# Optimization experiments

Measured on AMD Instinct MI355X. Metric: run time of the kernel, lower is better.

The kernel has to match this reference:

```python
import jax, jax.numpy as jnp
import numpy as np

B, S, D = 2, 2048, 2048
H, KVH = 16, 4
HD = D // H            # 128
KVD = KVH * HD         # 512
ROPE_BASE = 10000.0
EPS = 1e-6


def setup_inputs() -> dict:
    key = jax.random.key(0)
    k0, k1, k2, k3, k4, k5 = jax.random.split(key, 6)
    x = jax.random.normal(k0, (B, S, D), dtype=jnp.float32)
    # torch Linear weights are [out_features, in_features]
    Wq = jax.random.normal(k1, (D, D), dtype=jnp.float32) * 0.02
    Wk = jax.random.normal(k2, (KVD, D), dtype=jnp.float32) * 0.02
    Wv = jax.random.normal(k3, (KVD, D), dtype=jnp.float32) * 0.02
    Wproj = jax.random.normal(k4, (D, D), dtype=jnp.float32) * 0.02
    q_gain = jnp.ones((H,), dtype=jnp.float32)
    return {"x": x, "Wq": Wq, "Wk": Wk, "Wv": Wv, "Wproj": Wproj, "q_gain": q_gain}


def _rms_norm(t):
    return t * jax.lax.rsqrt(jnp.mean(t * t, axis=-1, keepdims=True) + EPS)


def _rope_tables(seqlen, dtype):
    half = HD // 2
    inv_freq = 1.0 / (ROPE_BASE ** (jnp.arange(0, HD, 2, dtype=jnp.float32) / HD))
    freqs = jnp.outer(jnp.arange(seqlen, dtype=jnp.float32), inv_freq)  # [S, half]
    return jnp.cos(freqs).astype(dtype)[None, None], jnp.sin(freqs).astype(dtype)[None, None]


def _apply_rope(t, cos, sin):
    half = t.shape[-1] // 2
    t1, t2 = t[..., :half], t[..., half:]
    return jnp.concatenate((t1 * cos + t2 * sin, -t1 * sin + t2 * cos), axis=-1)


def reference(x, Wq, Wk, Wv, Wproj, q_gain):
    bsz, seqlen, _ = x.shape
    # QKV projections (F.linear: x @ W.T)
    q = jnp.einsum('bsd,ed->bse', x, Wq).reshape(bsz, seqlen, H, HD).transpose(0, 2, 1, 3)
    k = jnp.einsum('bsd,ed->bse', x, Wk).reshape(bsz, seqlen, KVH, HD).transpose(0, 2, 1, 3)
    v = jnp.einsum('bsd,ed->bse', x, Wv).reshape(bsz, seqlen, KVH, HD).transpose(0, 2, 1, 3)
    # QK RMS-norm
    q = _rms_norm(q)
    k = _rms_norm(k)
    # RoPE
    cos, sin = _rope_tables(seqlen, q.dtype)
    q = _apply_rope(q, cos, sin)
    k = _apply_rope(k, cos, sin)
    # per-head query gain
    q = q * q_gain.astype(q.dtype)[None, :, None, None]
    # GQA: repeat_interleave kv heads
    rep = H // KVH
    k = jnp.repeat(k, rep, axis=1)
    v = jnp.repeat(v, rep, axis=1)
    # causal SDPA
    scale = 1.0 / jnp.sqrt(jnp.asarray(HD, dtype=q.dtype))
    scores = jnp.einsum('bhqd,bhkd->bhqk', q, k) * scale
    causal = jnp.tril(jnp.ones((seqlen, seqlen), dtype=bool))
    scores = jnp.where(causal[None, None], scores, jnp.finfo(scores.dtype).min)
    attn = jax.nn.softmax(scores, axis=-1)
    y = jnp.einsum('bhqk,bhkd->bhqd', attn, v)
    y = y.transpose(0, 2, 1, 3).reshape(bsz, seqlen, H * HD)
    return jnp.einsum('bse,de->bsd', y, Wproj)
```

## Files before the change

kernel.cpp:

```cpp
#include <hip/hip_runtime.h>


typedef __bf16 bf16x8 __attribute__((ext_vector_type(8)));
typedef float  f32x4  __attribute__((ext_vector_type(4)));
typedef float  f32x16 __attribute__((ext_vector_type(16)));

#define LOG2E 1.4426950408889634f
#define FIXC  16.59099297022308f

__device__ __forceinline__ float b2f(ushort h) {
  return __builtin_bit_cast(float, ((unsigned)h) << 16);
}
__device__ __forceinline__ ushort f2b(float f) {
  unsigned u = __builtin_bit_cast(unsigned, f);
  return (ushort)((u + 0x7fffu + ((u >> 16) & 1u)) >> 16);
}
__device__ __forceinline__ void async16(ushort* lds, const ushort* g) {
  __builtin_amdgcn_global_load_lds(
      (const __attribute__((address_space(1))) unsigned int*)(const void*)g,
      (__attribute__((address_space(3))) unsigned int*)(void*)lds, 16, 0, 0);
}
__device__ __forceinline__ f32x4 mfma16(bf16x8 a, bf16x8 b, f32x4 c) {
  return __builtin_amdgcn_mfma_f32_16x16x32_bf16(a, b, c, 0, 0, 0);
}
__device__ __forceinline__ f32x16 mfma32(bf16x8 a, bf16x8 b, f32x16 c) {
  return __builtin_amdgcn_mfma_f32_32x32x16_bf16(a, b, c, 0, 0, 0);
}

__global__ __launch_bounds__(256) void castk(const float* __restrict__ in,
                                             ushort* __restrict__ out) {
  int i = blockIdx.x * 256 + threadIdx.x;
  float4 v = ((const float4*)in)[i];
  ushort4 o = make_ushort4(f2b(v.x), f2b(v.y), f2b(v.z), f2b(v.w));
  ((ushort4*)out)[i] = o;
}

__global__ void rope_tables(float* __restrict__ cosT, float* __restrict__ sinT) {
  int s = blockIdx.x;
  int i = threadIdx.x;
  float invf = exp2f(-(float)i * (13.287712379549449f / 64.0f));
  float ang = (float)s * invf;
  float sn, cs;
  sincosf(ang, &sn, &cs);
  cosT[s * 64 + i] = cs;
  sinT[s * 64 + i] = sn;
}

__device__ __forceinline__ void store_c(float* C, size_t idx, float v) { C[idx] = v; }
__device__ __forceinline__ void store_c(ushort* C, size_t idx, float v) { C[idx] = f2b(v); }

template <typename TOUT>
__global__ __launch_bounds__(256) void gemm_bt(const ushort* __restrict__ A,
                                               const ushort* __restrict__ Bw,
                                               TOUT* __restrict__ C,
                                               int M, int N, int K) {
  __shared__ __align__(16) ushort As[128 * 64];
  __shared__ __align__(16) ushort Bs[128 * 64];
  int tid = threadIdx.x;
  int lane = tid & 63, wid = tid >> 6;
  int gx = gridDim.x;
  int nwg = gx * gridDim.y;
  int lid = blockIdx.y * gx + blockIdx.x;
  int cpx = nwg >> 3;
  int swz = (lid & 7) * cpx + (lid >> 3);
  int bm = swz / gx, bn = swz % gx;
  int wr = wid >> 1, wc = wid & 1;
  int lr = lane & 15, kg = lane >> 4;
  f32x4 z = {0.f, 0.f, 0.f, 0.f};
  f32x4 acc[4][4];
#pragma unroll
  for (int m = 0; m < 4; ++m)
#pragma unroll
    for (int n = 0; n < 4; ++n) acc[m][n] = z;

  const ushort* Ab = A + (size_t)bm * 128 * K;
  const ushort* Bb = Bw + (size_t)bn * 128 * K;

  for (int k0 = 0; k0 < K; k0 += 64) {
#pragma unroll
    for (int p = 0; p < 4; ++p) {
      int c = p * 256 + tid;
      int r = c >> 3, ch = c & 7;
      int chs = ch ^ (r & 7);
      async16(&As[c * 8], Ab + (size_t)r * K + k0 + chs * 8);
      async16(&Bs[c * 8], Bb + (size_t)r * K + k0 + chs * 8);
    }
    __syncthreads();
    bf16x8 af[4][2], bfr[4][2];
#pragma unroll
    for (int m = 0; m < 4; ++m)
#pragma unroll
      for (int kk = 0; kk < 2; ++kk) {
        int r = wr * 64 + m * 16 + lr;
        int a = (kk * 4 + kg) ^ (r & 7);
        af[m][kk] = *(const bf16x8*)&As[r * 64 + a * 8];
      }
#pragma unroll
    for (int n = 0; n < 4; ++n)
#pragma unroll
      for (int kk = 0; kk < 2; ++kk) {
        int r = wc * 64 + n * 16 + lr;
        int a = (kk * 4 + kg) ^ (r & 7);
        bfr[n][kk] = *(const bf16x8*)&Bs[r * 64 + a * 8];
      }
#pragma unroll
    for (int m = 0; m < 4; ++m)
#pragma unroll
      for (int n = 0; n < 4; ++n)
#pragma unroll
        for (int kk = 0; kk < 2; ++kk)
          acc[m][n] = mfma16(af[m][kk], bfr[n][kk], acc[m][n]);
    __syncthreads();
  }
#pragma unroll
  for (int m = 0; m < 4; ++m)
#pragma unroll
    for (int n = 0; n < 4; ++n)
#pragma unroll
      for (int r4 = 0; r4 < 4; ++r4) {
        int row = bm * 128 + wr * 64 + m * 16 + kg * 4 + r4;
        int col = bn * 128 + wc * 64 + n * 16 + lr;
        store_c(C, (size_t)row * N + col, acc[m][n][r4]);
      }
}

__global__ __launch_bounds__(256) void rms_rope(ushort* __restrict__ qkv,
                                                const float* __restrict__ gain,
                                                const float* __restrict__ cosT,
                                                const float* __restrict__ sinT) {
  int w = blockIdx.x * 4 + (threadIdx.x >> 6);
  int lane = threadIdx.x & 63;
  int token = w / 20, slot = w % 20;
  int s = token & 2047;
  ushort* p = qkv + (size_t)token * 3072 +
              (slot < 16 ? slot * 128 : 2048 + (slot - 16) * 128);
  float t1 = b2f(p[lane]);
  float t2 = b2f(p[lane + 64]);
  float ss = t1 * t1 + t2 * t2;
#pragma unroll
  for (int off = 32; off >= 1; off >>= 1) ss += __shfl_xor(ss, off);
  float r = rsqrtf(ss * (1.0f / 128.0f) + 1e-6f);
  t1 *= r; t2 *= r;
  float c = cosT[s * 64 + lane], sn = sinT[s * 64 + lane];
  float o1 = t1 * c + t2 * sn;
  float o2 = t2 * c - t1 * sn;
  if (slot < 16) {
    float g = gain[slot] * 0.08838834764831845f;
    o1 *= g; o2 *= g;
  }
  p[lane] = f2b(o1);
  p[lane + 64] = f2b(o2);
}

__global__ __launch_bounds__(256) void attn_fwd(const ushort* __restrict__ qkv,
                                                ushort* __restrict__ y) {
  __shared__ __align__(16) ushort LDS[32768];
  ushort* K0 = LDS;
  ushort* K1 = LDS + 8192;
  ushort* V0 = LDS + 16384;
  ushort* V1 = LDS + 24576;

  const int tid = threadIdx.x;
  const int lane = tid & 63;
  const int w = tid >> 6;
  const int hf = lane >> 5;
  const int lq = lane & 31;
  const int i = blockIdx.x, bh = blockIdx.y;
  const int b = bh >> 4, h = bh & 15, kvh = h >> 2;
  const int ta = i, tb = 31 - i;
  const size_t tokbase = (size_t)b * 2048;
  const bool isW01 = (w < 2);
  const int sub = isW01 ? w : (w - 2);

  const int kv0 = (tid & 15) * 4;
  const int d0 = (tid >> 4) * 8;

  union U16 { uint4 u; ushort s[8]; };
  U16 vA[4], vB[4];

  auto LOADV = [&](U16 (&vr)[4], int T) {
#pragma unroll
    for (int l = 0; l < 4; ++l)
      vr[l].u = *(const uint4*)(qkv + (tokbase + (size_t)T * 64 + kv0 + l) * 3072 +
                                2560 + kvh * 128 + d0);
  };
  auto WRITEV = [&](ushort* VB, U16 (&vr)[4]) {
#pragma unroll
    for (int j = 0; j < 8; ++j) {
      int row = d0 + j;
      int ad = row * 64 + ((((kv0 >> 3) ^ (row & 7)) << 3) | (kv0 & 7));
      *(ushort4*)&VB[ad] = make_ushort4(vr[0].s[j], vr[1].s[j], vr[2].s[j], vr[3].s[j]);
    }
  };
  auto STAGEK = [&](ushort* KB, int T) {
#pragma unroll
    for (int it = 0; it < 4; ++it) {
      int c = it * 256 + tid;
      int r = c >> 4, a = c & 15;
      int asrc = a ^ (r & 15);
      async16(&KB[c * 8],
              qkv + (tokbase + (size_t)T * 64 + r) * 3072 + 2048 + kvh * 128 + asrc * 8);
    }
  };

  bf16x8 qf[8];
  auto LOADQ = [&](int qrow0) {
#pragma unroll
    for (int kk = 0; kk < 8; ++kk)
      qf[kk] = *(const bf16x8*)(qkv + (tokbase + qrow0 + lq) * 3072 + h * 128 +
                                kk * 16 + hf * 8);
  };

  const f32x16 Z16 = {0.f,0.f,0.f,0.f,0.f,0.f,0.f,0.f,0.f,0.f,0.f,0.f,0.f,0.f,0.f,0.f};
  f32x16 acc[4];
#pragma unroll
  for (int db = 0; db < 4; ++db) acc[db] = Z16;
  float lsum = 0.f;

  auto COMPUTE = [&](const ushort* kb, const ushort* vt, bool domask, int kvbase, int qg) {
#pragma unroll
    for (int kvb = 0; kvb < 2; ++kvb) {
      f32x16 sc = Z16;
      __builtin_amdgcn_s_setprio(1);
#pragma unroll
      for (int kk = 0; kk < 8; ++kk) {
        int kv = kvb * 32 + lq;
        int ch = (2 * kk + hf) ^ (kv & 15);
        bf16x8 kf = *(const bf16x8*)&kb[kv * 128 + ch * 8];
        sc = mfma32(kf, qf[kk], sc);
      }
      __builtin_amdgcn_s_setprio(0);
      if (domask) {
#pragma unroll
        for (int r = 0; r < 16; ++r) {
          int kvl = (r & 3) + 8 * (r >> 2) + 4 * hf;
          if (kvbase + kvb * 32 + kvl > qg) sc[r] = -1.0e30f;
        }
      }
      float ex[16];
#pragma unroll
      for (int r = 0; r < 16; ++r) ex[r] = __shfl_xor(sc[r], 32);
#pragma unroll
      for (int c2 = 0; c2 < 2; ++c2) {
        bf16x8 pa;
#pragma unroll
        for (int j = 0; j < 8; ++j) {
          int r0 = 8 * c2 + (j & 3);
          int r1 = r0 + 4;
          float v0 = (j < 4) ? sc[r0] : ex[r0];
          float v1 = (j < 4) ? ex[r1] : sc[r1];
          float v = hf ? v1 : v0;
          float p = __builtin_amdgcn_exp2f(fmaf(v, LOG2E, -FIXC));
          lsum += p;
          pa[j] = __builtin_bit_cast(__bf16, f2b(p));
        }
        int kkpv = 2 * kvb + c2;
        __builtin_amdgcn_s_setprio(1);
#pragma unroll
        for (int db = 0; db < 4; ++db) {
          int d = db * 32 + lq;
          int ch = (2 * kkpv + hf) ^ (d & 7);
          bf16x8 vbf = *(const bf16x8*)&vt[d * 64 + ch * 8];
          acc[db] = mfma32(pa, vbf, acc[db]);
        }
        __builtin_amdgcn_s_setprio(0);
      }
    }
  };

  auto STOREO = [&](size_t rowbase, float lf) {
    float rl = 1.0f / lf;
#pragma unroll
    for (int r = 0; r < 16; ++r) {
      int q2 = (r & 3) + 8 * (r >> 2) + 4 * hf;
      float rlq = __shfl(rl, q2);
#pragma unroll
      for (int db = 0; db < 4; ++db) {
        int d = db * 32 + lq;
        y[(rowbase + q2) * 2048 + h * 128 + d] = f2b(acc[db][r] * rlq);
      }
    }
  };

  const int qrowA = (isW01 ? tb : ta) * 64 + sub * 32;
  const int qgA = qrowA + lq;
  LOADQ(qrowA);

  LOADV(vA, 0);
  STAGEK(K0, 0);
  WRITEV(V0, vA);
  __syncthreads();

  for (int t = 0; t <= ta; ++t) {
    ushort* kb = (t & 1) ? K1 : K0;
    ushort* vb = (t & 1) ? V1 : V0;
    bool more = (t < ta);
    if (more) {
      STAGEK((t & 1) ? K0 : K1, t + 1);
      LOADV(vA, t + 1);
    }
    COMPUTE(kb, vb, (!isW01 && t == ta), t * 64, qgA);
    if (more) WRITEV((t & 1) ? V0 : V1, vA);
    __syncthreads();
  }

  if (!isW01) {
    float lf = lsum + __shfl_xor(lsum, 32);
    STOREO(tokbase + (size_t)ta * 64 + sub * 32, lf);
#pragma unroll
    for (int db = 0; db < 4; ++db) acc[db] = Z16;
    lsum = 0.f;
    LOADQ(tb * 64 + sub * 32);
  }
  const int qgB = tb * 64 + sub * 32 + lq;

  {
    int t0 = ta + 1;
    bool h1 = (t0 + 1 <= tb);
    STAGEK(K0, t0);
    if (h1) STAGEK(K1, t0 + 1);
    LOADV(vA, t0);
    if (h1) LOADV(vB, t0 + 1);
    WRITEV(V0, vA);
    if (h1) WRITEV(V1, vB);
  }
  __syncthreads();

  for (int m = 0;; ++m) {
    int t0 = ta + 1 + 2 * m, t1 = t0 + 1;
    bool has1 = (t1 <= tb);
    bool morePairs = (t0 + 2 <= tb);
    bool more1 = (t0 + 3 <= tb);
    if (morePairs) {
      LOADV(vA, t0 + 2);
      if (more1) LOADV(vB, t0 + 3);
    }
    if (isW01) {
      COMPUTE(K0, V0, (t0 == tb), t0 * 64, qgB);
    } else if (has1) {
      COMPUTE(K1, V1, false, t1 * 64, qgB);
    }
    __syncthreads();
    if (!morePairs) break;
    STAGEK(K0, t0 + 2);
    if (more1) STAGEK(K1, t0 + 3);
    WRITEV(V0, vA);
    if (more1) WRITEV(V1, vB);
    __syncthreads();
  }

  float* scf = (float*)LDS;
  if (!isW01) {
    float lf = lsum + __shfl_xor(lsum, 32);
    int p = sub;
#pragma unroll
    for (int db = 0; db < 4; ++db)
#pragma unroll
      for (int r = 0; r < 16; ++r)
        scf[p * 4096 + (db * 16 + r) * 64 + lane] = acc[db][r];
    scf[8192 + p * 64 + lane] = lf;
  }
  __syncthreads();
  if (isW01) {
    int p = sub;
#pragma unroll
    for (int db = 0; db < 4; ++db)
#pragma unroll
      for (int r = 0; r < 16; ++r)
        acc[db][r] += scf[p * 4096 + (db * 16 + r) * 64 + lane];
    float lf = lsum + __shfl_xor(lsum, 32) + scf[8192 + p * 64 + lane];
    STOREO(tokbase + (size_t)tb * 64 + sub * 32, lf);
  }
}

extern "C" void kernel_launch(void* const* d_in, const int* in_sizes, int n_in,
                              void* d_out, int out_size, void* d_ws, size_t ws_size,
                              hipStream_t stream) {
  const float* x  = (const float*)d_in[0];
  const float* Wq = (const float*)d_in[1];
  const float* Wk = (const float*)d_in[2];
  const float* Wv = (const float*)d_in[3];
  const float* Wp = (const float*)d_in[4];
  const float* qg = (const float*)d_in[5];
  float* out = (float*)d_out;

  char* w = (char*)d_ws;
  ushort* xb    = (ushort*)w; w += (size_t)4096 * 2048 * 2;
  ushort* wqkv  = (ushort*)w; w += (size_t)3072 * 2048 * 2;
  ushort* wproj = (ushort*)w; w += (size_t)2048 * 2048 * 2;
  ushort* qkv   = (ushort*)w; w += (size_t)4096 * 3072 * 2;
  ushort* yb    = (ushort*)w; w += (size_t)4096 * 2048 * 2;
  float*  cosT  = (float*)w;  w += (size_t)2048 * 64 * 4;
  float*  sinT  = (float*)w;  w += (size_t)2048 * 64 * 4;

  castk<<<8192, 256, 0, stream>>>(x, xb);
  castk<<<4096, 256, 0, stream>>>(Wq, wqkv);
  castk<<<1024, 256, 0, stream>>>(Wk, wqkv + (size_t)2048 * 2048);
  castk<<<1024, 256, 0, stream>>>(Wv, wqkv + (size_t)2560 * 2048);
  castk<<<4096, 256, 0, stream>>>(Wp, wproj);
  rope_tables<<<2048, 64, 0, stream>>>(cosT, sinT);

  gemm_bt<ushort><<<dim3(24, 32), 256, 0, stream>>>(xb, wqkv, qkv, 4096, 3072, 2048);
  rms_rope<<<20480, 256, 0, stream>>>(qkv, qg, cosT, sinT);
  attn_fwd<<<dim3(16, 32), 256, 0, stream>>>(qkv, yb);
  gemm_bt<float><<<dim3(16, 32), 256, 0, stream>>>(yb, wproj, out, 4096, 2048, 2048);
}
```

Baseline: 377.3 us.

## Split attention KV tile across wave pairs with 512-thread blocks

Attention blocks grow from 4 to 8 waves. Each pair of waves shares the same query rows and splits every 64-key tile into two 32-key halves. The partial accumulators and row sums are then combined through LDS in a multi-stage reduction before the output is written. The goal is more wave-level parallelism and latency hiding per block on a grid of only 512 blocks, at the cost of extra LDS reductions, more barriers, and higher register pressure under launch_bounds(512,4).

New measurement: 442.2 us. +17.2%, slower.

```diff
diff --git a/kernel.cpp b/kernel.cpp
--- a/kernel.cpp
+++ b/kernel.cpp
@@ -152,50 +152,51 @@
   p[lane + 64] = f2b(o2);
 }
 
-__global__ __launch_bounds__(256) void attn_fwd(const ushort* __restrict__ qkv,
-                                                ushort* __restrict__ y) {
-  __shared__ __align__(16) ushort LDS[32768];
+__global__ __launch_bounds__(512, 4) void attn_fwd(const ushort* __restrict__ qkv,
+                                                   ushort* __restrict__ y) {
+  __shared__ __align__(16) ushort LDS[34816];
   ushort* K0 = LDS;
   ushort* K1 = LDS + 8192;
   ushort* V0 = LDS + 16384;
   ushort* V1 = LDS + 24576;
+  float* scl = (float*)(LDS + 32768);
 
   const int tid = threadIdx.x;
   const int lane = tid & 63;
   const int w = tid >> 6;
+  const int rg = w >> 1;
+  const int hf2 = w & 1;
+  const int kvofs = hf2 * 32;
   const int hf = lane >> 5;
   const int lq = lane & 31;
-  const int i = blockIdx.x, bh = blockIdx.y;
+  const int pairi = blockIdx.x, bh = blockIdx.y;
   const int b = bh >> 4, h = bh & 15, kvh = h >> 2;
-  const int ta = i, tb = 31 - i;
+  const int ta = pairi, tb = 31 - pairi;
   const size_t tokbase = (size_t)b * 2048;
-  const bool isW01 = (w < 2);
-  const int sub = isW01 ? w : (w - 2);
-
-  const int kv0 = (tid & 15) * 4;
-  const int d0 = (tid >> 4) * 8;
-
+
+  const int kv0 = (tid & 31) * 2;
+  const int d0v = (tid >> 5) * 8;
   union U16 { uint4 u; ushort s[8]; };
-  U16 vA[4], vB[4];
-
-  auto LOADV = [&](U16 (&vr)[4], int T) {
-#pragma unroll
-    for (int l = 0; l < 4; ++l)
-      vr[l].u = *(const uint4*)(qkv + (tokbase + (size_t)T * 64 + kv0 + l) * 3072 +
-                                2560 + kvh * 128 + d0);
-  };
-  auto WRITEV = [&](ushort* VB, U16 (&vr)[4]) {
+  U16 vA[2];
+
+  auto LOADV = [&](int T) {
+#pragma unroll
+    for (int l = 0; l < 2; ++l)
+      vA[l].u = *(const uint4*)(qkv + (tokbase + (size_t)T * 64 + kv0 + l) * 3072 +
+                                2560 + kvh * 128 + d0v);
+  };
+  auto WRITEV = [&](ushort* VB) {
 #pragma unroll
     for (int j = 0; j < 8; ++j) {
-      int row = d0 + j;
-      int ad = row * 64 + ((((kv0 >> 3) ^ (row & 7)) << 3) | (kv0 & 7));
-      *(ushort4*)&VB[ad] = make_ushort4(vr[0].s[j], vr[1].s[j], vr[2].s[j], vr[3].s[j]);
+      int row = d0v + j;
+      int ad = row * 64 + (((((kv0 >> 3) ^ (row & 7)) << 3)) | (kv0 & 7));
+      *(ushort2*)&VB[ad] = make_ushort2(vA[0].s[j], vA[1].s[j]);
     }
   };
   auto STAGEK = [&](ushort* KB, int T) {
 #pragma unroll
-    for (int it = 0; it < 4; ++it) {
-      int c = it * 256 + tid;
+    for (int it = 0; it < 2; ++it) {
+      int c = it * 512 + tid;
       int r = c >> 4, a = c & 15;
       int asrc = a ^ (r & 15);
       async16(&KB[c * 8],
@@ -204,12 +205,14 @@
   };
 
   bf16x8 qf[8];
-  auto LOADQ = [&](int qrow0) {
+  int qrow = (rg < 2 ? tb : ta) * 64 + (rg & 1) * 32;
+  auto LOADQ = [&]() {
 #pragma unroll
     for (int kk = 0; kk < 8; ++kk)
-      qf[kk] = *(const bf16x8*)(qkv + (tokbase + qrow0 + lq) * 3072 + h * 128 +
+      qf[kk] = *(const bf16x8*)(qkv + (tokbase + qrow + lq) * 3072 + h * 128 +
                                 kk * 16 + hf * 8);
   };
+  LOADQ();
 
   const f32x16 Z16 = {0.f,0.f,0.f,0.f,0.f,0.f,0.f,0.f,0.f,0.f,0.f,0.f,0.f,0.f,0.f,0.f};
   f32x16 acc[4];
@@ -217,58 +220,69 @@
   for (int db = 0; db < 4; ++db) acc[db] = Z16;
   float lsum = 0.f;
 
-  auto COMPUTE = [&](const ushort* kb, const ushort* vt, bool domask, int kvbase, int qg) {
-#pragma unroll
-    for (int kvb = 0; kvb < 2; ++kvb) {
-      f32x16 sc = Z16;
+  auto COMPUTE = [&](const ushort* kb, const ushort* vt, bool domask, int tile) {
+    int qg = qrow + lq;
+    f32x16 sc = Z16;
+    __builtin_amdgcn_s_setprio(1);
+#pragma unroll
+    for (int kk = 0; kk < 8; ++kk) {
+      int kv = kvofs + lq;
+      int ch = (2 * kk + hf) ^ (kv & 15);
+      bf16x8 kf = *(const bf16x8*)&kb[kv * 128 + ch * 8];
+      sc = mfma32(kf, qf[kk], sc);
+    }
+    __builtin_amdgcn_s_setprio(0);
+    if (domask) {
+#pragma unroll
+      for (int r = 0; r < 16; ++r) {
+        int kvl = (r & 3) + 8 * (r >> 2) + 4 * hf;
+        if (tile * 64 + kvofs + kvl > qg) sc[r] = -1.0e30f;
+      }
+    }
+#pragma unroll
+    for (int c2 = 0; c2 < 2; ++c2) {
+      float ex[8];
+#pragma unroll
+      for (int rr = 0; rr < 8; ++rr) ex[rr] = __shfl_xor(sc[8 * c2 + rr], 32);
+      bf16x8 pa;
+#pragma unroll
+      for (int j = 0; j < 8; ++j) {
+        int r0 = 8 * c2 + (j & 3);
+        int r1 = r0 + 4;
+        float v = hf ? ((j < 4) ? ex[(j & 3) + 4] : sc[r1])
+                     : ((j < 4) ? sc[r0] : ex[j & 3]);
+        float p = __builtin_amdgcn_exp2f(fmaf(v, LOG2E, -FIXC));
+        lsum += p;
+        pa[j] = __builtin_bit_cast(__bf16, f2b(p));
+      }
+      int kkpv = 2 * hf2 + c2;
       __builtin_amdgcn_s_setprio(1);
 #pragma unroll
-      for (int kk = 0; kk < 8; ++kk) {
-        int kv = kvb * 32 + lq;
-        int ch = (2 * kk + hf) ^ (kv & 15);
-        bf16x8 kf = *(const bf16x8*)&kb[kv * 128 + ch * 8];
-        sc = mfma32(kf, qf[kk], sc);
+      for (int db = 0; db < 4; ++db) {
+        int d = db * 32 + lq;
+        int ch = (2 * kkpv + hf) ^ (d & 7);
+        bf16x8 vbf = *(const bf16x8*)&vt[d * 64 + ch * 8];
+        acc[db] = mfma32(pa, vbf, acc[db]);
       }
       __builtin_amdgcn_s_setprio(0);
-      if (domask) {
-#pragma unroll
-        for (int r = 0; r < 16; ++r) {
-          int kvl = (r & 3) + 8 * (r >> 2) + 4 * hf;
-          if (kvbase + kvb * 32 + kvl > qg) sc[r] = -1.0e30f;
-        }
-      }
-      float ex[16];
-#pragma unroll
-      for (int r = 0; r < 16; ++r) ex[r] = __shfl_xor(sc[r], 32);
-#pragma unroll
-      for (int c2 = 0; c2 < 2; ++c2) {
-        bf16x8 pa;
-#pragma unroll
-        for (int j = 0; j < 8; ++j) {
-          int r0 = 8 * c2 + (j & 3);
-          int r1 = r0 + 4;
-          float v0 = (j < 4) ? sc[r0] : ex[r0];
-          float v1 = (j < 4) ? ex[r1] : sc[r1];
-          float v = hf ? v1 : v0;
-          float p = __builtin_amdgcn_exp2f(fmaf(v, LOG2E, -FIXC));
-          lsum += p;
-          pa[j] = __builtin_bit_cast(__bf16, f2b(p));
-        }
-        int kkpv = 2 * kvb + c2;
-        __builtin_amdgcn_s_setprio(1);
-#pragma unroll
-        for (int db = 0; db < 4; ++db) {
-          int d = db * 32 + lq;
-          int ch = (2 * kkpv + hf) ^ (d & 7);
-          bf16x8 vbf = *(const bf16x8*)&vt[d * 64 + ch * 8];
-          acc[db] = mfma32(pa, vbf, acc[db]);
-        }
-        __builtin_amdgcn_s_setprio(0);
-      }
-    }
-  };
-
-  auto STOREO = [&](size_t rowbase, float lf) {
+    }
+  };
+
+  auto DUMP = [&](int r) {
+    float* rp = (float*)((char*)LDS + r * 16384);
+#pragma unroll
+    for (int db = 0; db < 4; ++db)
+#pragma unroll
+      for (int q = 0; q < 16; ++q) rp[(db * 16 + q) * 64 + lane] = acc[db][q];
+  };
+  auto ADDIN = [&](int r) {
+    float* rp = (float*)((char*)LDS + r * 16384);
+#pragma unroll
+    for (int db = 0; db < 4; ++db)
+#pragma unroll
+      for (int q = 0; q < 16; ++q) acc[db][q] += rp[(db * 16 + q) * 64 + lane];
+  };
+  auto STOREO = [&](float lf) {
     float rl = 1.0f / lf;
 #pragma unroll
     for (int r = 0; r < 16; ++r) {
@@ -277,52 +291,56 @@
 #pragma unroll
       for (int db = 0; db < 4; ++db) {
         int d = db * 32 + lq;
-        y[(rowbase + q2) * 2048 + h * 128 + d] = f2b(acc[db][r] * rlq);
-      }
-    }
-  };
-
-  const int qrowA = (isW01 ? tb : ta) * 64 + sub * 32;
-  const int qgA = qrowA + lq;
-  LOADQ(qrowA);
-
-  LOADV(vA, 0);
+        y[(tokbase + qrow + q2) * 2048 + h * 128 + d] = f2b(acc[db][r] * rlq);
+      }
+    }
+  };
+
   STAGEK(K0, 0);
-  WRITEV(V0, vA);
+  LOADV(0);
+  WRITEV(V0);
   __syncthreads();
 
   for (int t = 0; t <= ta; ++t) {
-    ushort* kb = (t & 1) ? K1 : K0;
-    ushort* vb = (t & 1) ? V1 : V0;
+    const ushort* kb = (t & 1) ? K1 : K0;
+    const ushort* vb = (t & 1) ? V1 : V0;
     bool more = (t < ta);
     if (more) {
       STAGEK((t & 1) ? K0 : K1, t + 1);
-      LOADV(vA, t + 1);
-    }
-    COMPUTE(kb, vb, (!isW01 && t == ta), t * 64, qgA);
-    if (more) WRITEV((t & 1) ? V0 : V1, vA);
+      LOADV(t + 1);
+    }
+    COMPUTE(kb, vb, (w >= 4 && t == ta), t);
+    if (more) WRITEV((t & 1) ? V0 : V1);
     __syncthreads();
   }
 
-  if (!isW01) {
-    float lf = lsum + __shfl_xor(lsum, 32);
-    STOREO(tokbase + (size_t)ta * 64 + sub * 32, lf);
+  bool hasT1 = (ta + 2 <= tb);
+  if (w == 5 || w == 7) {
+    DUMP(w == 5 ? 2 : 3);
+    scl[(w == 5 ? 0 : 1) * 64 + lane] = lsum;
+  }
+  STAGEK(K0, ta + 1);
+  if (hasT1) STAGEK(K1, ta + 2);
+  LOADV(ta + 1);
+  __syncthreads();
+  if (w == 4 || w == 6) {
+    ADDIN(w == 4 ? 2 : 3);
+    float lf = lsum + scl[(w == 4 ? 0 : 1) * 64 + lane];
+    lf = lf + __shfl_xor(lf, 32);
+    STOREO(lf);
+  }
+  if (w >= 4) {
 #pragma unroll
     for (int db = 0; db < 4; ++db) acc[db] = Z16;
     lsum = 0.f;
-    LOADQ(tb * 64 + sub * 32);
-  }
-  const int qgB = tb * 64 + sub * 32 + lq;
-
-  {
-    int t0 = ta + 1;
-    bool h1 = (t0 + 1 <= tb);
-    STAGEK(K0, t0);
-    if (h1) STAGEK(K1, t0 + 1);
-    LOADV(vA, t0);
-    if (h1) LOADV(vB, t0 + 1);
-    WRITEV(V0, vA);
-    if (h1) WRITEV(V1, vB);
+    qrow = tb * 64 + (rg & 1) * 32;
+    LOADQ();
+  }
+  __syncthreads();
+  WRITEV(V0);
+  if (hasT1) {
+    LOADV(ta + 2);
+    WRITEV(V1);
   }
   __syncthreads();
 
@@ -330,46 +348,45 @@
     int t0 = ta + 1 + 2 * m, t1 = t0 + 1;
     bool has1 = (t1 <= tb);
     bool morePairs = (t0 + 2 <= tb);
-    bool more1 = (t0 + 3 <= tb);
-    if (morePairs) {
-      LOADV(vA, t0 + 2);
-      if (more1) LOADV(vB, t0 + 3);
-    }
-    if (isW01) {
-      COMPUTE(K0, V0, (t0 == tb), t0 * 64, qgB);
+    bool more1 = (t1 + 2 <= tb);
+    if (morePairs) LOADV(t0 + 2);
+    if (rg < 2) {
+      COMPUTE(K0, V0, (t0 == tb), t0);
     } else if (has1) {
-      COMPUTE(K1, V1, false, t1 * 64, qgB);
+      COMPUTE(K1, V1, false, t1);
     }
     __syncthreads();
     if (!morePairs) break;
     STAGEK(K0, t0 + 2);
-    if (more1) STAGEK(K1, t0 + 3);
-    WRITEV(V0, vA);
-    if (more1) WRITEV(V1, vB);
+    WRITEV(V0);
+    if (more1) {
+      STAGEK(K1, t1 + 2);
+      LOADV(t1 + 2);
+      WRITEV(V1);
+    }
     __syncthreads();
   }
 
-  float* scf = (float*)LDS;
-  if (!isW01) {
-    float lf = lsum + __shfl_xor(lsum, 32);
-    int p = sub;
-#pragma unroll
-    for (int db = 0; db < 4; ++db)
-#pragma unroll
-      for (int r = 0; r < 16; ++r)
-        scf[p * 4096 + (db * 16 + r) * 64 + lane] = acc[db][r];
-    scf[8192 + p * 64 + lane] = lf;
-  }
-  __syncthreads();
-  if (isW01) {
-    int p = sub;
-#pragma unroll
-    for (int db = 0; db < 4; ++db)
-#pragma unroll
-      for (int r = 0; r < 16; ++r)
-        acc[db][r] += scf[p * 4096 + (db * 16 + r) * 64 + lane];
-    float lf = lsum + __shfl_xor(lsum, 32) + scf[8192 + p * 64 + lane];
-    STOREO(tokbase + (size_t)tb * 64 + sub * 32, lf);
+  if (w & 1) {
+    DUMP(w >> 1);
+    scl[(w >> 1) * 64 + lane] = lsum;
+  }
+  __syncthreads();
+  if (!(w & 1)) {
+    ADDIN(w >> 1);
+    lsum += scl[(w >> 1) * 64 + lane];
+  }
+  __syncthreads();
+  if (w == 4 || w == 6) {
+    DUMP(w == 4 ? 0 : 1);
+    scl[(w == 4 ? 0 : 1) * 64 + lane] = lsum;
+  }
+  __syncthreads();
+  if (w == 0 || w == 2) {
+    ADDIN(w == 0 ? 0 : 1);
+    float lf = lsum + scl[(w == 0 ? 0 : 1) * 64 + lane];
+    lf = lf + __shfl_xor(lf, 32);
+    STOREO(lf);
   }
 }
 
@@ -402,6 +419,6 @@
 
   gemm_bt<ushort><<<dim3(24, 32), 256, 0, stream>>>(xb, wqkv, qkv, 4096, 3072, 2048);
   rms_rope<<<20480, 256, 0, stream>>>(qkv, qg, cosT, sinT);
-  attn_fwd<<<dim3(16, 32), 256, 0, stream>>>(qkv, yb);
+  attn_fwd<<<dim3(16, 32), 512, 0, stream>>>(qkv, yb);
   gemm_bt<float><<<dim3(16, 32), 256, 0, stream>>>(yb, wproj, out, 4096, 2048, 2048);
 }
```
